# Kernel tuning notes

Measured on AMD Instinct MI355X. Metric: run time of the kernel, lower is better.

The kernel has to match this reference:

```python
import jax, jax.numpy as jnp
import numpy as np

D_MODEL = 1024
STATE_DIM = 16
BATCH = 32
SEQ = 2048


def setup_inputs() -> dict:
    key = jax.random.key(0)
    k_x, k_win, k_bin, k_wout, k_bout = jax.random.split(key, 5)
    proj_dim = 2 * D_MODEL + 3 * STATE_DIM
    x = jax.random.normal(k_x, (BATCH, SEQ, D_MODEL), dtype=jnp.float32)
    # Dense kernels (glorot-ish scale) and zero biases, as in fresh keras layers
    W_in = jax.random.normal(k_win, (D_MODEL, proj_dim), dtype=jnp.float32) * 0.02
    b_in = jnp.zeros((proj_dim,), dtype=jnp.float32)
    W_out = jax.random.normal(k_wout, (D_MODEL, D_MODEL), dtype=jnp.float32) * 0.02
    b_out = jnp.zeros((D_MODEL,), dtype=jnp.float32)
    # A_log init: -log([1..state_dim])
    A_log = -jnp.log(jnp.arange(1, STATE_DIM + 1, dtype=jnp.float32))
    return {"x": x, "W_in": W_in, "b_in": b_in, "A_log": A_log,
            "W_out": W_out, "b_out": b_out}


def _selective_scan(delta, A, B, C):
    # delta, B, C: [b, s, n]; A: [n]
    # state_t = exp(A * delta_t) * state_{t-1} + B_t ; y_t = sum(state_t * C_t)
    def step(state, inp):
        delta_t, B_t, C_t = inp  # each [b, n]
        state = jnp.exp(A * delta_t) * state + B_t
        y = jnp.sum(state * C_t, axis=-1)  # [b]
        return state, y

    b = delta.shape[0]
    init = jnp.zeros((b, A.shape[0]), dtype=delta.dtype)
    # scan over time: move seq axis to front -> [s, b, n]
    xs = (jnp.swapaxes(delta, 0, 1), jnp.swapaxes(B, 0, 1), jnp.swapaxes(C, 0, 1))
    _, ys = jax.lax.scan(step, init, xs)  # ys: [s, b]
    return jnp.swapaxes(ys, 0, 1)  # [b, s]


def reference(x, W_in, b_in, A_log, W_out, b_out):
    xz = jnp.einsum('bsd,dp->bsp', x, W_in) + b_in  # [b, s, 2*d + 3*n]
    d, n = D_MODEL, STATE_DIM
    xm = xz[..., :d]                     # unused by scan (matches original)
    z = xz[..., d:2 * d]                 # [b, s, d]
    Bm = xz[..., 2 * d:2 * d + n]        # [b, s, n]
    Cm = xz[..., 2 * d + n:2 * d + 2 * n]
    delta = jax.nn.softplus(xz[..., 2 * d + 2 * n:])  # [b, s, n]
    A = -jnp.exp(A_log)                  # [n]
    y = _selective_scan(delta, A, Bm, Cm)  # [b, s]
    y = y[..., None] * jax.nn.gelu(z, approximate=False)  # [b, s, d]
    return jnp.einsum('bsd,de->bse', y, W_out) + b_out
```

## Files before the change

kernel.cpp:

```cpp
#include <hip/hip_runtime.h>
#include <cstdint>

typedef float fx4 __attribute__((ext_vector_type(4)));
typedef short sx8 __attribute__((ext_vector_type(8)));
typedef short sx4 __attribute__((ext_vector_type(4)));

#define NSTATE 16
#define SEQ_LEN 2048
#define NBATCH 32
#define MROWS 65536
#define KDIM 1024
#define N1 1072
#define N1PAD 1152
#define BK 32
#define NSTEP (KDIM / BK)
#define TILE_SHORTS 4096
#define TSTRIDE (NSTEP * TILE_SHORTS)
#define RING 4
#define SLOT_SHORTS 8192

__device__ __forceinline__ short f2bf(float f) {
  unsigned u = __float_as_uint(f);
  u += 0x7FFFu + ((u >> 16) & 1u);
  return (short)(u >> 16);
}

__device__ __forceinline__ float gelu_exact(float x) {
  float ax = fabsf(x) * 0.70710678118654752f;
  float t = __builtin_amdgcn_rcpf(fmaf(0.3275911f, ax, 1.0f));
  float p = fmaf(1.061405429f, t, -1.453152027f);
  p = fmaf(p, t, 1.421413741f);
  p = fmaf(p, t, -0.284496736f);
  p = fmaf(p, t, 0.254829592f);
  p = p * t;
  float e = __expf(-ax * ax);
  float erfv = fmaf(-p, e, 1.0f);
  erfv = copysignf(erfv, x);
  return 0.5f * x * (1.0f + erfv);
}

#define GLOAD_LDS16(gp, lp)                                                          \
  __builtin_amdgcn_global_load_lds(                                                  \
      (const __attribute__((address_space(1))) unsigned int*)(gp),                   \
      (__attribute__((address_space(3))) unsigned int*)(lp), 16, 0, 0)

#define SBAR() do { __builtin_amdgcn_s_barrier(); asm volatile("" ::: "memory"); } while (0)

__global__ void convert_pack_x(const float* __restrict__ x, short* __restrict__ xbp) {
  const int wave = threadIdx.x >> 6;
  const int lane = threadIdx.x & 63;
  const int r0 = blockIdx.x * 64 + wave * 16;
  const int q = (lane & 7) >> 1;
  const int eo = (lane & 1) * 4;
  const int kt0 = lane >> 3;
  for (int r16 = 0; r16 < 16; ++r16) {
    const int m = r0 + r16;
    const int rloc = m & 127;
    const long pbase = ((long)(m >> 7) * NSTEP) * TILE_SHORTS + rloc * 32;
    const int p8 = (((q + (rloc >> 1)) & 3)) * 8 + eo;
#pragma unroll
    for (int seg = 0; seg < 4; ++seg) {
      fx4 v = *(const fx4*)(x + (long)m * KDIM + seg * 256 + lane * 4);
      sx4 o;
      o[0] = f2bf(v[0]); o[1] = f2bf(v[1]); o[2] = f2bf(v[2]); o[3] = f2bf(v[3]);
      *(sx4*)(xbp + pbase + (long)(seg * 8 + kt0) * TILE_SHORTS + p8) = o;
    }
  }
}

__global__ void transpose_w_kernel(const float* __restrict__ src, short* __restrict__ dst,
                                   int src_cols, int col_off, int valid_rows) {
  __shared__ float t[32][33];
  int j0 = blockIdx.x * 32;
  int k0 = blockIdx.y * 32;
  int c = threadIdx.x & 31;
  int r = threadIdx.x >> 5;
#pragma unroll
  for (int i = 0; i < 4; i++) {
    int k = k0 + r + i * 8;
    int j = j0 + c;
    float v = (j < valid_rows) ? src[(long)k * src_cols + col_off + j] : 0.f;
    t[r + i * 8][c] = v;
  }
  __syncthreads();
#pragma unroll
  for (int i = 0; i < 4; i++) {
    int n = j0 + r + i * 8;
    int k = k0 + c;
    int rr = n & 127;
    long addr = ((long)(n >> 7) * NSTEP + (k >> 5)) * TILE_SHORTS + rr * 32
              + ((((k >> 3) & 3) + ((rr >> 1) & 3)) & 3) * 8 + (k & 7);
    dst[addr] = f2bf(t[c][r + i * 8]);
  }
}

__device__ __forceinline__ void gemm_mainloop256(const short* __restrict__ Abase,
                                                 const short* __restrict__ Bbase,
                                                 short* lds, fx4 acc[4][4]) {
  const int tid = threadIdx.x;
  const int lane = tid & 63;
  const int wave = tid >> 6;
  const int wm = wave >> 2, wn = wave & 3;
  const int l15 = lane & 15, ks = lane >> 4;

#pragma unroll
  for (int i = 0; i < 4; i++)
#pragma unroll
    for (int j = 0; j < 4; j++) acc[i][j] = fx4{0.f, 0.f, 0.f, 0.f};

  short* AshR = lds;
  short* BshR = lds + RING * SLOT_SHORTS;
  const short* Asrc = Abase + (long)(tid >> 9) * TSTRIDE + (tid & 511) * 8;
  const short* Bsrc = Bbase + (long)(tid >> 9) * TSTRIDE + (tid & 511) * 8;
  const int dst = tid * 8;

  const int rslot = ((ks + (l15 >> 1)) & 3) * 8;
  const int aoff = (wm >> 1) * TILE_SHORTS + ((wm & 1) * 64 + l15) * 32 + rslot;
  const int boff = (wn >> 1) * TILE_SHORTS + ((wn & 1) * 64 + l15) * 32 + rslot;

#pragma unroll
  for (int s = 0; s < RING - 1; s++) {
    GLOAD_LDS16(Asrc + (long)s * TILE_SHORTS, AshR + s * SLOT_SHORTS + dst);
    GLOAD_LDS16(Bsrc + (long)s * TILE_SHORTS, BshR + s * SLOT_SHORTS + dst);
  }

  for (int s = 0; s < NSTEP; ++s) {
    const int rem = NSTEP - 1 - s;
    if (rem >= 2)      asm volatile("s_waitcnt vmcnt(4)" ::: "memory");
    else if (rem == 1) asm volatile("s_waitcnt vmcnt(2)" ::: "memory");
    else               asm volatile("s_waitcnt vmcnt(0)" ::: "memory");
    SBAR();

    if (s + 3 < NSTEP) {
      const int sl = (s + 3) & (RING - 1);
      GLOAD_LDS16(Asrc + (long)(s + 3) * TILE_SHORTS, AshR + sl * SLOT_SHORTS + dst);
      GLOAD_LDS16(Bsrc + (long)(s + 3) * TILE_SHORTS, BshR + sl * SLOT_SHORTS + dst);
    }

    const short* sa = AshR + (s & (RING - 1)) * SLOT_SHORTS + aoff;
    const short* sb = BshR + (s & (RING - 1)) * SLOT_SHORTS + boff;
    sx8 af[4], bfr[4];
#pragma unroll
    for (int i = 0; i < 4; i++) af[i] = *(const sx8*)(sa + i * 512);
#pragma unroll
    for (int j = 0; j < 4; j++) bfr[j] = *(const sx8*)(sb + j * 512);

    __builtin_amdgcn_s_setprio(1);
#pragma unroll
    for (int i = 0; i < 4; i++)
#pragma unroll
      for (int j = 0; j < 4; j++)
        acc[i][j] = __builtin_amdgcn_mfma_f32_16x16x32_bf16(af[i], bfr[j], acc[i][j], 0, 0, 0);
    __builtin_amdgcn_s_setprio(0);
  }
}

__global__ __launch_bounds__(1024, 1) void gemm1_kernel(
    const short* __restrict__ xbp, const short* __restrict__ Wt1p,
    const float* __restrict__ b_in, short* __restrict__ g) {
  extern __shared__ short lds[];
  const int bid = blockIdx.x;
  const int wgid = (bid & 7) * 128 + (bid >> 3);
  const int nt = wgid & 3;
  const int mt = wgid >> 2;
  fx4 acc[4][4];
  gemm_mainloop256(xbp + (long)(mt * 2) * TSTRIDE,
                   Wt1p + (long)(nt * 2) * TSTRIDE, lds, acc);

  const int lane = threadIdx.x & 63;
  const int wave = threadIdx.x >> 6;
  const int wm = wave >> 2, wn = wave & 3;
  const int m0 = mt * 256;
  const int n0 = nt * 256;

#pragma unroll
  for (int ni = 0; ni < 4; ni++) {
    int n = n0 + wn * 64 + ni * 16 + (lane & 15);
    float bias = b_in[1024 + n];
#pragma unroll
    for (int mi = 0; mi < 4; mi++) {
#pragma unroll
      for (int r = 0; r < 4; r++) {
        int m = m0 + wm * 64 + mi * 16 + (lane >> 4) * 4 + r;
        float v = acc[mi][ni][r] + bias;
        int rr = m & 127;
        long addr = ((long)(m >> 7) * NSTEP + (n >> 5)) * TILE_SHORTS + rr * 32
                  + ((((n >> 3) & 3) + ((rr >> 1) & 3)) & 3) * 8 + (n & 7);
        g[addr] = f2bf(gelu_exact(v));
      }
    }
  }
}

__global__ __launch_bounds__(256, 2) void gemm_bcd_kernel(
    const short* __restrict__ xbp, const short* __restrict__ Wt1p,
    const float* __restrict__ b_in, const float* __restrict__ A_log,
    float* __restrict__ Bb, float* __restrict__ Cb, float* __restrict__ ab) {
  __shared__ short Ash[3 * 4096] __attribute__((aligned(16)));
  __shared__ short Bsh[3 * 2048] __attribute__((aligned(16)));
  const int tid = threadIdx.x;
  const int lane = tid & 63, wave = tid >> 6;
  const int l15 = lane & 15, ks = lane >> 4;
  const int bid = blockIdx.x;
  const int mt = (bid & 7) * 64 + (bid >> 3);
  const short* Abase = xbp + (long)mt * TSTRIDE;
  const short* Bbase = Wt1p + (long)8 * TSTRIDE;

  fx4 acc[2][3];
#pragma unroll
  for (int i = 0; i < 2; i++)
#pragma unroll
    for (int j = 0; j < 3; j++) acc[i][j] = fx4{0.f, 0.f, 0.f, 0.f};

  const int rslot = ((ks + (l15 >> 1)) & 3) * 8;
  const int aofb = (wave * 32 + l15) * 32 + rslot;

#pragma unroll
  for (int s = 0; s < 2; s++) {
    GLOAD_LDS16(Abase + (long)s * TILE_SHORTS + tid * 8, Ash + s * 4096 + tid * 8);
    GLOAD_LDS16(Abase + (long)s * TILE_SHORTS + 2048 + tid * 8, Ash + s * 4096 + 2048 + tid * 8);
    GLOAD_LDS16(Bbase + (long)s * TILE_SHORTS + tid * 8, Bsh + s * 2048 + tid * 8);
  }

  for (int s = 0; s < NSTEP; ++s) {
    if (s < NSTEP - 1) asm volatile("s_waitcnt vmcnt(3)" ::: "memory");
    else               asm volatile("s_waitcnt vmcnt(0)" ::: "memory");
    SBAR();
    if (s + 2 < NSTEP) {
      const int sl = (s + 2) % 3;
      GLOAD_LDS16(Abase + (long)(s + 2) * TILE_SHORTS + tid * 8, Ash + sl * 4096 + tid * 8);
      GLOAD_LDS16(Abase + (long)(s + 2) * TILE_SHORTS + 2048 + tid * 8, Ash + sl * 4096 + 2048 + tid * 8);
      GLOAD_LDS16(Bbase + (long)(s + 2) * TILE_SHORTS + tid * 8, Bsh + sl * 2048 + tid * 8);
    }
    const short* sa = Ash + (s % 3) * 4096 + aofb;
    const short* sb = Bsh + (s % 3) * 2048;
    sx8 af[2], bfr[3];
#pragma unroll
    for (int i = 0; i < 2; i++) af[i] = *(const sx8*)(sa + i * 512);
#pragma unroll
    for (int j = 0; j < 3; j++) bfr[j] = *(const sx8*)(sb + (j * 16 + l15) * 32 + rslot);
#pragma unroll
    for (int i = 0; i < 2; i++)
#pragma unroll
      for (int j = 0; j < 3; j++)
        acc[i][j] = __builtin_amdgcn_mfma_f32_16x16x32_bf16(af[i], bfr[j], acc[i][j], 0, 0, 0);
  }

  const float biasB = b_in[2048 + l15];
  const float biasC = b_in[2064 + l15];
  const float biasD = b_in[2080 + l15];
  const float Ac = -expf(A_log[l15]);
#pragma unroll
  for (int mi = 0; mi < 2; mi++) {
#pragma unroll
    for (int r = 0; r < 4; r++) {
      int m = mt * 128 + wave * 32 + mi * 16 + (lane >> 4) * 4 + r;
      Bb[m * NSTATE + l15] = acc[mi][0][r] + biasB;
      Cb[m * NSTATE + l15] = acc[mi][1][r] + biasC;
      float v = acc[mi][2][r] + biasD;
      float dlt = (v > 20.f) ? v : log1pf(expf(v));
      ab[m * NSTATE + l15] = expf(Ac * dlt);
    }
  }
}

__global__ void scan_kernel(const float* __restrict__ ab, const float* __restrict__ Bb,
                            const float* __restrict__ Cb, float* __restrict__ y) {
  __shared__ float Ash[16][17], Bsh[16][17];
  const int b = blockIdx.x;
  const int tid = threadIdx.x;
  const int seg = tid >> 4, ch = tid & 15;
  const long base = ((long)b * SEQ_LEN + seg * 128) * NSTATE + ch;
  const float* pa = ab + base;
  const float* pb = Bb + base;
  const float* pc = Cb + base;

  float A = 1.f, Bc = 0.f;
  for (int i0 = 0; i0 < 128; i0 += 8) {
    float av[8], bv[8];
#pragma unroll
    for (int u = 0; u < 8; u++) { av[u] = pa[(i0 + u) * NSTATE]; bv[u] = pb[(i0 + u) * NSTATE]; }
#pragma unroll
    for (int u = 0; u < 8; u++) { Bc = fmaf(av[u], Bc, bv[u]); A *= av[u]; }
  }
  Ash[seg][ch] = A; Bsh[seg][ch] = Bc;
  __syncthreads();

  if (tid < 16) {
    float s = 0.f;
    for (int sg = 0; sg < 16; ++sg) {
      float nxt = fmaf(Ash[sg][tid], s, Bsh[sg][tid]);
      Bsh[sg][tid] = s;
      s = nxt;
    }
  }
  __syncthreads();

  float s = Bsh[seg][ch];
  float* py = y + (long)b * SEQ_LEN + seg * 128;
  for (int i0 = 0; i0 < 128; i0 += 8) {
    float av[8], bv[8], cv[8];
#pragma unroll
    for (int u = 0; u < 8; u++) {
      av[u] = pa[(i0 + u) * NSTATE];
      bv[u] = pb[(i0 + u) * NSTATE];
      cv[u] = pc[(i0 + u) * NSTATE];
    }
#pragma unroll
    for (int u = 0; u < 8; u++) {
      s = fmaf(av[u], s, bv[u]);
      float p = s * cv[u];
      p += __shfl_xor(p, 1);
      p += __shfl_xor(p, 2);
      p += __shfl_xor(p, 4);
      p += __shfl_xor(p, 8);
      if (ch == 0) py[i0 + u] = p;
    }
  }
}

__global__ __launch_bounds__(1024, 1) void gemm2_kernel(
    const short* __restrict__ g, const short* __restrict__ Wt2p,
    const float* __restrict__ y, const float* __restrict__ b_out,
    float* __restrict__ out) {
  extern __shared__ short lds[];
  const int bid = blockIdx.x;
  const int wgid = (bid & 7) * 128 + (bid >> 3);
  const int nt = wgid & 3;
  const int mt = wgid >> 2;
  fx4 acc[4][4];
  gemm_mainloop256(g + (long)(mt * 2) * TSTRIDE,
                   Wt2p + (long)(nt * 2) * TSTRIDE, lds, acc);

  const int lane = threadIdx.x & 63;
  const int wave = threadIdx.x >> 6;
  const int wm = wave >> 2, wn = wave & 3;
  const int m0 = mt * 256;
  const int n0 = nt * 256;

#pragma unroll
  for (int mi = 0; mi < 4; mi++) {
#pragma unroll
    for (int r = 0; r < 4; r++) {
      int m = m0 + wm * 64 + mi * 16 + (lane >> 4) * 4 + r;
      float ym = y[m];
#pragma unroll
      for (int ni = 0; ni < 4; ni++) {
        int n = n0 + wn * 64 + ni * 16 + (lane & 15);
        out[(long)m * 1024 + n] = fmaf(ym, acc[mi][ni][r], b_out[n]);
      }
    }
  }
}

extern "C" void kernel_launch(void* const* d_in, const int* in_sizes, int n_in,
                              void* d_out, int out_size, void* d_ws, size_t ws_size,
                              hipStream_t stream) {
  const float* x     = (const float*)d_in[0];
  const float* W_in  = (const float*)d_in[1];
  const float* b_in  = (const float*)d_in[2];
  const float* A_log = (const float*)d_in[3];
  const float* W_out = (const float*)d_in[4];
  const float* b_out = (const float*)d_in[5];
  float* out = (float*)d_out;

  char* ws = (char*)d_ws;
  short* xbp = (short*)ws;  ws += (size_t)MROWS * KDIM * 2;
  short* g   = (short*)ws;  ws += (size_t)MROWS * KDIM * 2;
  short* Wt1p = (short*)ws; ws += (size_t)N1PAD * KDIM * 2;
  short* Wt2p = (short*)ws; ws += (size_t)KDIM * KDIM * 2;
  float* Bb = (float*)ws;  ws += (size_t)MROWS * NSTATE * 4;
  float* Cb = (float*)ws;  ws += (size_t)MROWS * NSTATE * 4;
  float* ab = (float*)ws;  ws += (size_t)MROWS * NSTATE * 4;
  float* y  = (float*)ws;  ws += (size_t)MROWS * 4;

  const int ldsBytes = 2 * RING * SLOT_SHORTS * 2;

  convert_pack_x<<<1024, 256, 0, stream>>>(x, xbp);
  transpose_w_kernel<<<dim3(N1PAD / 32, 32), 256, 0, stream>>>(W_in, Wt1p, 2096, 1024, N1);
  transpose_w_kernel<<<dim3(32, 32), 256, 0, stream>>>(W_out, Wt2p, 1024, 0, 1024);
  gemm_bcd_kernel<<<512, 256, 0, stream>>>(xbp, Wt1p, b_in, A_log, Bb, Cb, ab);
  scan_kernel<<<NBATCH, 256, 0, stream>>>(ab, Bb, Cb, y);
  gemm1_kernel<<<1024, 1024, ldsBytes, stream>>>(xbp, Wt1p, b_in, g);
  gemm2_kernel<<<1024, 1024, ldsBytes, stream>>>(g, Wt2p, y, b_out, out);
}
```

Before: 484.9 us.

## Rewrite gemm2 mainloop as 512-thread, 8-phase double-buffered pipeline with BK=64

Replaces the shared 1024-thread ring-buffer mainloop in gemm2 with a custom 512-thread loop. Each wave now computes a 128x64 tile using 32 accumulators. K steps of 64 are double-buffered in LDS, and the global-to-LDS loads for the next step are interleaved between four MFMA phases, with s_setprio raising priority around the MFMA work. The goal is better MFMA utilization and more data reuse per wave. The cost is higher register pressure and many more barriers per iteration.

```diff
diff --git a/kernel.cpp b/kernel.cpp
--- a/kernel.cpp
+++ b/kernel.cpp
@@ -14,10 +14,12 @@
 #define N1PAD 1152
 #define BK 32
 #define NSTEP (KDIM / BK)
+#define NT64 (KDIM / 64)
 #define TILE_SHORTS 4096
 #define TSTRIDE (NSTEP * TILE_SHORTS)
 #define RING 4
 #define SLOT_SHORTS 8192
+#define DBUF_SHORTS 32768
 
 __device__ __forceinline__ short f2bf(float f) {
   unsigned u = __float_as_uint(f);
@@ -45,6 +47,8 @@
       (__attribute__((address_space(3))) unsigned int*)(lp), 16, 0, 0)
 
 #define SBAR() do { __builtin_amdgcn_s_barrier(); asm volatile("" ::: "memory"); } while (0)
+#define LGKM0() asm volatile("s_waitcnt lgkmcnt(0)" ::: "memory")
+#define VMCNT0() asm volatile("s_waitcnt vmcnt(0)" ::: "memory")
 
 __global__ void convert_pack_x(const float* __restrict__ x, short* __restrict__ xbp) {
   const int wave = threadIdx.x >> 6;
@@ -319,7 +323,7 @@
   }
 }
 
-__global__ __launch_bounds__(1024, 1) void gemm2_kernel(
+__global__ __launch_bounds__(512, 1) void gemm2_kernel(
     const short* __restrict__ g, const short* __restrict__ Wt2p,
     const float* __restrict__ y, const float* __restrict__ b_out,
     float* __restrict__ out) {
@@ -328,21 +332,140 @@
   const int wgid = (bid & 7) * 128 + (bid >> 3);
   const int nt = wgid & 3;
   const int mt = wgid >> 2;
-  fx4 acc[4][4];
-  gemm_mainloop256(g + (long)(mt * 2) * TSTRIDE,
-                   Wt2p + (long)(nt * 2) * TSTRIDE, lds, acc);
-
-  const int lane = threadIdx.x & 63;
-  const int wave = threadIdx.x >> 6;
+  const short* Abase = g + (long)(mt * 2) * TSTRIDE;
+  const short* Bbase = Wt2p + (long)(nt * 2) * TSTRIDE;
+
+  const int tid = threadIdx.x;
+  const int lane = tid & 63;
+  const int wave = tid >> 6;
   const int wm = wave >> 2, wn = wave & 3;
+  const int l15 = lane & 15, ks = lane >> 4;
+
+  fx4 acc[8][4];
+#pragma unroll
+  for (int i = 0; i < 8; i++)
+#pragma unroll
+    for (int j = 0; j < 4; j++) acc[i][j] = fx4{0.f, 0.f, 0.f, 0.f};
+
+  const int dst = tid * 8;
+  const int rslot = ((ks + (l15 >> 1)) & 3) * 8;
+  int aof[8][2], bof[4][2];
+#pragma unroll
+  for (int mi = 0; mi < 8; mi++)
+#pragma unroll
+    for (int c = 0; c < 2; c++)
+      aof[mi][c] = wm * 8192 + c * 4096 + (mi * 16 + l15) * 32 + rslot;
+#pragma unroll
+  for (int ni = 0; ni < 4; ni++)
+#pragma unroll
+    for (int c = 0; c < 2; c++)
+      bof[ni][c] = 16384 + (wn >> 1) * 8192 + c * 4096 + ((wn & 1) * 64 + ni * 16 + l15) * 32 + rslot;
+
+#define STAGE_A(t, buf)                                                                  \
+  do {                                                                                   \
+    GLOAD_LDS16(Abase + (long)(2 * (t)) * TILE_SHORTS + dst,              (buf) + dst);  \
+    GLOAD_LDS16(Abase + (long)(2 * (t) + 1) * TILE_SHORTS + dst,          (buf) + 4096 + dst); \
+    GLOAD_LDS16(Abase + TSTRIDE + (long)(2 * (t)) * TILE_SHORTS + dst,    (buf) + 8192 + dst); \
+    GLOAD_LDS16(Abase + TSTRIDE + (long)(2 * (t) + 1) * TILE_SHORTS + dst,(buf) + 12288 + dst); \
+  } while (0)
+#define STAGE_B(t, buf)                                                                  \
+  do {                                                                                   \
+    GLOAD_LDS16(Bbase + (long)(2 * (t)) * TILE_SHORTS + dst,              (buf) + 16384 + dst); \
+    GLOAD_LDS16(Bbase + (long)(2 * (t) + 1) * TILE_SHORTS + dst,          (buf) + 20480 + dst); \
+    GLOAD_LDS16(Bbase + TSTRIDE + (long)(2 * (t)) * TILE_SHORTS + dst,    (buf) + 24576 + dst); \
+    GLOAD_LDS16(Bbase + TSTRIDE + (long)(2 * (t) + 1) * TILE_SHORTS + dst,(buf) + 28672 + dst); \
+  } while (0)
+
+  STAGE_A(0, lds);
+  STAGE_B(0, lds);
+  VMCNT0();
+  SBAR();
+
+  for (int t = 0; t < NT64; ++t) {
+    const short* cur = lds + (t & 1) * DBUF_SHORTS;
+    short* nxt = lds + ((t + 1) & 1) * DBUF_SHORTS;
+    const bool st = (t + 1) < NT64;
+    sx8 a03[4][2], a47[4][2], b01[2][2], b23[2][2];
+
+#pragma unroll
+    for (int mi = 0; mi < 4; mi++)
+#pragma unroll
+      for (int c = 0; c < 2; c++) a03[mi][c] = *(const sx8*)(cur + aof[mi][c]);
+#pragma unroll
+    for (int ni = 0; ni < 2; ni++)
+#pragma unroll
+      for (int c = 0; c < 2; c++) b01[ni][c] = *(const sx8*)(cur + bof[ni][c]);
+    if (st) STAGE_A(t + 1, nxt);
+    SBAR();
+    LGKM0();
+    __builtin_amdgcn_s_setprio(1);
+#pragma unroll
+    for (int mi = 0; mi < 4; mi++)
+#pragma unroll
+      for (int ni = 0; ni < 2; ni++)
+#pragma unroll
+        for (int c = 0; c < 2; c++)
+          acc[mi][ni] = __builtin_amdgcn_mfma_f32_16x16x32_bf16(a03[mi][c], b01[ni][c], acc[mi][ni], 0, 0, 0);
+    __builtin_amdgcn_s_setprio(0);
+    SBAR();
+
+#pragma unroll
+    for (int ni = 0; ni < 2; ni++)
+#pragma unroll
+      for (int c = 0; c < 2; c++) b23[ni][c] = *(const sx8*)(cur + bof[2 + ni][c]);
+    if (st) STAGE_B(t + 1, nxt);
+    SBAR();
+    LGKM0();
+    __builtin_amdgcn_s_setprio(1);
+#pragma unroll
+    for (int mi = 0; mi < 4; mi++)
+#pragma unroll
+      for (int ni = 0; ni < 2; ni++)
+#pragma unroll
+        for (int c = 0; c < 2; c++)
+          acc[mi][2 + ni] = __builtin_amdgcn_mfma_f32_16x16x32_bf16(a03[mi][c], b23[ni][c], acc[mi][2 + ni], 0, 0, 0);
+    __builtin_amdgcn_s_setprio(0);
+    SBAR();
+
+#pragma unroll
+    for (int mi = 0; mi < 4; mi++)
+#pragma unroll
+      for (int c = 0; c < 2; c++) a47[mi][c] = *(const sx8*)(cur + aof[4 + mi][c]);
+    SBAR();
+    LGKM0();
+    __builtin_amdgcn_s_setprio(1);
+#pragma unroll
+    for (int mi = 0; mi < 4; mi++)
+#pragma unroll
+      for (int ni = 0; ni < 2; ni++)
+#pragma unroll
+        for (int c = 0; c < 2; c++)
+          acc[4 + mi][ni] = __builtin_amdgcn_mfma_f32_16x16x32_bf16(a47[mi][c], b01[ni][c], acc[4 + mi][ni], 0, 0, 0);
+    __builtin_amdgcn_s_setprio(0);
+    SBAR();
+
+    __builtin_amdgcn_s_setprio(1);
+#pragma unroll
+    for (int mi = 0; mi < 4; mi++)
+#pragma unroll
+      for (int ni = 0; ni < 2; ni++)
+#pragma unroll
+        for (int c = 0; c < 2; c++)
+          acc[4 + mi][2 + ni] = __builtin_amdgcn_mfma_f32_16x16x32_bf16(a47[mi][c], b23[ni][c], acc[4 + mi][2 + ni], 0, 0, 0);
+    __builtin_amdgcn_s_setprio(0);
+    VMCNT0();
+    SBAR();
+  }
+#undef STAGE_A
+#undef STAGE_B
+
   const int m0 = mt * 256;
   const int n0 = nt * 256;
-
-#pragma unroll
-  for (int mi = 0; mi < 4; mi++) {
+#pragma unroll
+  for (int mi = 0; mi < 8; mi++) {
 #pragma unroll
     for (int r = 0; r < 4; r++) {
-      int m = m0 + wm * 64 + mi * 16 + (lane >> 4) * 4 + r;
+      int m = m0 + wm * 128 + mi * 16 + (lane >> 4) * 4 + r;
       float ym = y[m];
 #pragma unroll
       for (int ni = 0; ni < 4; ni++) {
@@ -374,13 +497,14 @@
   float* ab = (float*)ws;  ws += (size_t)MROWS * NSTATE * 4;
   float* y  = (float*)ws;  ws += (size_t)MROWS * 4;
 
-  const int ldsBytes = 2 * RING * SLOT_SHORTS * 2;
+  const int ldsRing = 2 * RING * SLOT_SHORTS * 2;
+  const int lds8ph  = 2 * DBUF_SHORTS * 2;
 
   convert_pack_x<<<1024, 256, 0, stream>>>(x, xbp);
   transpose_w_kernel<<<dim3(N1PAD / 32, 32), 256, 0, stream>>>(W_in, Wt1p, 2096, 1024, N1);
   transpose_w_kernel<<<dim3(32, 32), 256, 0, stream>>>(W_out, Wt2p, 1024, 0, 1024);
   gemm_bcd_kernel<<<512, 256, 0, stream>>>(xbp, Wt1p, b_in, A_log, Bb, Cb, ab);
   scan_kernel<<<NBATCH, 256, 0, stream>>>(ab, Bb, Cb, y);
-  gemm1_kernel<<<1024, 1024, ldsBytes, stream>>>(xbp, Wt1p, b_in, g);
-  gemm2_kernel<<<1024, 1024, ldsBytes, stream>>>(g, Wt2p, y, b_out, out);
-}
+  gemm1_kernel<<<1024, 1024, ldsRing, stream>>>(xbp, Wt1p, b_in, g);
+  gemm2_kernel<<<1024, 512, lds8ph, stream>>>(g, Wt2p, y, b_out, out);
+}
```

Result: slower. 500.7 us (+3.3%).
